# Optimization experiments

Hardware: AMD Instinct MI355X
Metric: run time of the kernel (lower is better)

Reference implementation:

```python
import jax, jax.numpy as jnp
import numpy as np

NEG_SLOPE = 0.2


def gat_conv(x, src, dst, W, att_src, att_dst, bias, heads, out_ch, concat):
    """PyG-style GATConv (eval mode, self-loops already appended to src/dst)."""
    N = x.shape[0]
    h = (x @ W).reshape(N, heads, out_ch)                      # [N,H,C]
    a_src = jnp.einsum('nhc,hc->nh', h, att_src)               # [N,H]
    a_dst = jnp.einsum('nhc,hc->nh', h, att_dst)               # [N,H]
    e = jax.nn.leaky_relu(a_src[src] + a_dst[dst], NEG_SLOPE)  # [E,H]
    # numerically-stable softmax segmented by destination node
    emax = jax.ops.segment_max(e, dst, num_segments=N)         # [N,H]
    e = jnp.exp(e - emax[dst])
    denom = jax.ops.segment_sum(e, dst, num_segments=N)
    alpha = e / (denom[dst] + 1e-16)                           # [E,H]
    msg = h[src] * alpha[..., None]                            # [E,H,C]
    out = jax.ops.segment_sum(msg, dst, num_segments=N)        # [N,H,C]
    out = out.reshape(N, heads * out_ch) if concat else out.mean(axis=1)
    return out + bias


def setup_inputs() -> dict:
    key = jax.random.key(0)
    ks = jax.random.split(key, 9)
    N, E, IN, OUT = 100000, 1600000, 128, 40
    H1, C1 = 8, 8
    x = jax.random.normal(ks[0], (N, IN), dtype=jnp.float32)
    edge_index = jax.random.randint(ks[1], (2, E), 0, N, dtype=jnp.int64)
    s = 0.1
    return {
        'x': x,
        'edge_index': edge_index,
        'W1': jax.random.normal(ks[2], (IN, H1 * C1), dtype=jnp.float32) * s,
        'att_src1': jax.random.normal(ks[3], (H1, C1), dtype=jnp.float32) * s,
        'att_dst1': jax.random.normal(ks[4], (H1, C1), dtype=jnp.float32) * s,
        'b1': jnp.zeros((H1 * C1,), dtype=jnp.float32),
        'W2': jax.random.normal(ks[5], (H1 * C1, OUT), dtype=jnp.float32) * s,
        'att_src2': jax.random.normal(ks[6], (1, OUT), dtype=jnp.float32) * s,
        'att_dst2': jax.random.normal(ks[7], (1, OUT), dtype=jnp.float32) * s,
        'b2': jnp.zeros((OUT,), dtype=jnp.float32),
    }


def reference(x, edge_index, W1, att_src1, att_dst1, b1, W2, att_src2, att_dst2, b2):
    N = x.shape[0]
    loops = jnp.arange(N, dtype=edge_index.dtype)
    src = jnp.concatenate([edge_index[0], loops])  # self-loops (PyG default)
    dst = jnp.concatenate([edge_index[1], loops])
    h = gat_conv(x, src, dst, W1, att_src1, att_dst1, b1, 8, 8, True)
    h = jax.nn.elu(h)  # dropout is identity in eval mode
    out = gat_conv(h, src, dst, W2, att_src2, att_dst2, b2, 1, W2.shape[1], False)
    return jax.nn.log_softmax(out, axis=-1)
```

## Files before the change

kernel.cpp:

```cpp
#include <hip/hip_runtime.h>
#include <math.h>

#define NEG_SLOPE 0.2f
#define BSHIFT 8
#define MAXBUK 512

typedef __attribute__((ext_vector_type(8))) short short8;
typedef __attribute__((ext_vector_type(4))) float floatx4;

static __device__ __forceinline__ float lrelu_exp(float e) {
    e = fmaxf(e, NEG_SLOPE * e);
    return __expf(e);
}

static __device__ __forceinline__ short f2bf(float f) {
    union { float f; unsigned u; } v; v.f = f;
    unsigned r = v.u + 0x7FFFu + ((v.u >> 16) & 1u);
    return (short)(r >> 16);
}
static __device__ __forceinline__ float bf2f(unsigned short s) {
    union { float f; unsigned u; } v;
    v.u = ((unsigned)s) << 16;
    return v.f;
}
static __device__ __forceinline__ float bfpair_lo(unsigned v) {
    union { float f; unsigned u; } x; x.u = v << 16; return x.f;
}
static __device__ __forceinline__ float bfpair_hi(unsigned v) {
    union { float f; unsigned u; } x; x.u = v & 0xffff0000u; return x.f;
}
static __device__ __forceinline__ void splitbf(float f, short& hi, short& lo) {
    hi = f2bf(f);
    lo = f2bf(f - bf2f((unsigned short)hi));
}


__global__ __launch_bounds__(512) void k_hist(const int* __restrict__ dst, int E, int CHUNK,
                                              int NBLK, int NBUK, int* __restrict__ blockhist) {
    __shared__ int hist[MAXBUK];
    int t = threadIdx.x, b = blockIdx.x;
    for (int i = t; i < NBUK; i += 512) hist[i] = 0;
    __syncthreads();
    int e0 = b * CHUNK, e1 = e0 + CHUNK; if (e1 > E) e1 = E;
    for (int e = e0 + t; e < e1; e += 512) atomicAdd(&hist[dst[e] >> BSHIFT], 1);
    __syncthreads();
    for (int i = t; i < NBUK; i += 512) blockhist[(size_t)i * NBLK + b] = hist[i];
}

__global__ __launch_bounds__(256) void k_colscan(int* __restrict__ blockhist,
                                                 int* __restrict__ btot, int NBLK) {
    int bucket = blockIdx.x, t = threadIdx.x;
    int lane = t & 63, wv = t >> 6;
    __shared__ int wsum[4];
    __shared__ int carry_s;
    if (t == 0) carry_s = 0;
    __syncthreads();
    for (int base = 0; base < NBLK; base += 256) {
        int idx = base + t;
        int v = (idx < NBLK) ? blockhist[(size_t)bucket * NBLK + idx] : 0;
        int s = v;
#pragma unroll
        for (int o = 1; o < 64; o <<= 1) {
            int u = __shfl_up(s, o, 64);
            if (lane >= o) s += u;
        }
        if (lane == 63) wsum[wv] = s;
        __syncthreads();
        int b0 = 0;
#pragma unroll
        for (int w = 0; w < 4; ++w) b0 += (w < wv) ? wsum[w] : 0;
        int excl = s + b0 - v + carry_s;
        if (idx < NBLK) blockhist[(size_t)bucket * NBLK + idx] = excl;
        __syncthreads();
        if (t == 255) carry_s += s + b0;
        __syncthreads();
    }
    if (t == 0) btot[bucket] = carry_s;
}

__global__ __launch_bounds__(512) void k_bucket_scan(const int* __restrict__ btot,
                                                     int* __restrict__ bucketbase, int NBUK) {
    __shared__ int sh[512];
    int t = threadIdx.x;
    int v = (t < NBUK) ? btot[t] : 0;
    sh[t] = v;
    __syncthreads();
#pragma unroll
    for (int o = 1; o < 512; o <<= 1) {
        int u = (t >= o) ? sh[t - o] : 0;
        __syncthreads();
        sh[t] += u;
        __syncthreads();
    }
    if (t < NBUK) bucketbase[t] = sh[t] - v;
    if (t == NBUK - 1) bucketbase[NBUK] = sh[t];
}

__global__ __launch_bounds__(512) void k_partition(const int* __restrict__ src,
                                                   const int* __restrict__ dst, int E, int CHUNK,
                                                   int NBLK, int NBUK,
                                                   const int* __restrict__ blockhist,
                                                   const int* __restrict__ bucketbase,
                                                   unsigned* __restrict__ packed) {
    __shared__ int cur[MAXBUK];
    int t = threadIdx.x, b = blockIdx.x;
    for (int i = t; i < NBUK; i += 512)
        cur[i] = blockhist[(size_t)i * NBLK + b] + bucketbase[i];
    __syncthreads();
    int e0 = b * CHUNK, e1 = e0 + CHUNK; if (e1 > E) e1 = E;
    for (int e = e0 + t; e < e1; e += 512) {
        int d = dst[e], s = src[e];
        int pos = atomicAdd(&cur[d >> BSHIFT], 1);
        packed[pos] = ((unsigned)s << 8) | ((unsigned)d & 255u);
    }
}

__global__ __launch_bounds__(256) void k_fine(const unsigned* __restrict__ packed,
                                              const int* __restrict__ bucketbase,
                                              int* __restrict__ offsets,
                                              int* __restrict__ csr_src,
                                              int N, int NBUK) {
    __shared__ int fcnt[256];
    __shared__ int wsum[4];
    int bucket = blockIdx.x, t = threadIdx.x;
    int lo = bucket << BSHIFT;
    int nn = N - lo; if (nn > 256) nn = 256;
    int ebase = bucketbase[bucket];
    int ecnt = bucketbase[bucket + 1] - ebase;
    fcnt[t] = 0;
    __syncthreads();
    for (int i = t; i < ecnt; i += 256) {
        unsigned p = packed[ebase + i];
        atomicAdd(&fcnt[p & 255u], 1);
    }
    __syncthreads();
    int v = fcnt[t];
    int lane = t & 63, wv = t >> 6;
    int s = v;
#pragma unroll
    for (int o = 1; o < 64; o <<= 1) {
        int u = __shfl_up(s, o, 64);
        if (lane >= o) s += u;
    }
    if (lane == 63) wsum[wv] = s;
    __syncthreads();
    int base = 0;
#pragma unroll
    for (int w = 0; w < 4; ++w) base += (w < wv) ? wsum[w] : 0;
    int excl = s + base - v;
    if (t < nn) offsets[lo + t] = ebase + excl;
    if (bucket == NBUK - 1 && t == 0) offsets[N] = ebase + ecnt;
    __syncthreads();
    fcnt[t] = excl;
    __syncthreads();
    for (int i = t; i < ecnt; i += 256) {
        unsigned p = packed[ebase + i];
        int pos = atomicAdd(&fcnt[p & 255u], 1);
        csr_src[ebase + pos] = (int)(p >> 8);
    }
}

__global__ __launch_bounds__(256) void k_splitW2(const float* __restrict__ W2,
                                                 short* __restrict__ w2h,
                                                 short* __restrict__ w2l) {
    int i = blockIdx.x * 256 + threadIdx.x;
    if (i < 64 * 48) {
        int row = i / 48, col = i % 48;
        short hi = 0, lo = 0;
        if (col < 40) splitbf(W2[row * 40 + col], hi, lo);
        w2h[i] = hi; w2l[i] = lo;
    }
}

__global__ __launch_bounds__(256) void k_gemm1(const float* __restrict__ x,
                                               const float* __restrict__ W1,
                                               const float* __restrict__ att_s,
                                               const float* __restrict__ att_d,
                                               unsigned short* __restrict__ h1b,
                                               float* __restrict__ a_s1,
                                               float* __restrict__ a_d1, int N) {
    int tid = threadIdx.x, wave = tid >> 6, lane = tid & 63;
    int n16 = lane & 15, q = lane >> 4;
    int nb = blockIdx.x * 64 + wave * 16;
    if (nb >= N) return;

    short8 bfr[4][4];
#pragma unroll
    for (int ct = 0; ct < 4; ++ct) {
        int n = ct * 16 + n16;
#pragma unroll
        for (int kc = 0; kc < 4; ++kc) {
            int k0 = kc * 32 + q * 8;
            short8 b;
#pragma unroll
            for (int j = 0; j < 8; ++j) b[j] = f2bf(W1[(k0 + j) * 64 + n]);
            bfr[ct][kc] = b;
        }
    }

    int arow = nb + n16; if (arow >= N) arow = N - 1;
    const float* xr = x + (size_t)arow * 128 + q * 8;
    short8 afr[4];
#pragma unroll
    for (int kc = 0; kc < 4; ++kc) {
        float4 u0 = *(const float4*)(xr + kc * 32);
        float4 u1 = *(const float4*)(xr + kc * 32 + 4);
        short8 a;
        a[0] = f2bf(u0.x); a[1] = f2bf(u0.y); a[2] = f2bf(u0.z); a[3] = f2bf(u0.w);
        a[4] = f2bf(u1.x); a[5] = f2bf(u1.y); a[6] = f2bf(u1.z); a[7] = f2bf(u1.w);
        afr[kc] = a;
    }

    floatx4 acc[4];
#pragma unroll
    for (int ct = 0; ct < 4; ++ct) {
        floatx4 c = {0.f, 0.f, 0.f, 0.f};
#pragma unroll
        for (int kc = 0; kc < 4; ++kc)
            c = __builtin_amdgcn_mfma_f32_16x16x32_bf16(afr[kc], bfr[ct][kc], c, 0, 0, 0);
        acc[ct] = c;
    }

#pragma unroll
    for (int ct = 0; ct < 4; ++ct) {
#pragma unroll
        for (int r = 0; r < 4; ++r) {
            int row = nb + q * 4 + r;
            if (row < N) h1b[(size_t)row * 64 + ct * 16 + n16] = (unsigned short)f2bf(acc[ct][r]);
        }
    }

#pragma unroll
    for (int ct = 0; ct < 4; ++ct) {
        float as = att_s[ct * 16 + n16];
        float ad = att_d[ct * 16 + n16];
#pragma unroll
        for (int r = 0; r < 4; ++r) {
            float ps = acc[ct][r] * as;
            float pd = acc[ct][r] * ad;
#pragma unroll
            for (int m = 1; m < 8; m <<= 1) {
                ps += __shfl_xor(ps, m, 64);
                pd += __shfl_xor(pd, m, 64);
            }
            int row = nb + q * 4 + r;
            if ((n16 & 7) == 0 && row < N) {
                int h = 2 * ct + (n16 >> 3);
                a_s1[row * 8 + h] = ps;
                a_d1[row * 8 + h] = pd;
            }
        }
    }
}

__global__ __launch_bounds__(256) void k_agg1(const unsigned short* __restrict__ h1b,
                                              const float* __restrict__ a_s1,
                                              const float* __restrict__ a_d1,
                                              const int* __restrict__ offsets,
                                              const int* __restrict__ csr_src,
                                              const float* __restrict__ b1,
                                              float* __restrict__ y1, int N) {
    int wave = threadIdx.x >> 6, lane = threadIdx.x & 63;
    int q = lane >> 4;
    int ll = lane & 15;
    int d = (blockIdx.x * 4 + wave) * 4 + q;
    bool dvalid = (d < N);
    int de = dvalid ? d : N - 1;
    int g = ll >> 3;
    int c = ll & 7;
    float ad = a_d1[de * 8 + c];
    int i0 = offsets[de];
    int deg = dvalid ? (offsets[de + 1] - i0) : 0;
    int dmax = deg;
    dmax = max(dmax, __shfl_xor(dmax, 16, 64));
    dmax = max(dmax, __shfl_xor(dmax, 32, 64));
    float acc[8] = {0.f, 0.f, 0.f, 0.f, 0.f, 0.f, 0.f, 0.f};
    float wsum_l = 0.f;
    if (g == 0) {
        float w0 = lrelu_exp(a_s1[de * 8 + c] + ad);
        uint4 v = *(const uint4*)(h1b + (size_t)de * 64 + 8 * c);
        acc[0] = w0 * bfpair_lo(v.x); acc[1] = w0 * bfpair_hi(v.x);
        acc[2] = w0 * bfpair_lo(v.y); acc[3] = w0 * bfpair_hi(v.y);
        acc[4] = w0 * bfpair_lo(v.z); acc[5] = w0 * bfpair_hi(v.z);
        acc[6] = w0 * bfpair_lo(v.w); acc[7] = w0 * bfpair_hi(v.w);
        wsum_l = w0;
    }
    for (int j = 0; j < dmax; j += 8) {
        int b0 = i0 + j + 4 * g;
        int idx[4]; bool lv[4];
#pragma unroll
        for (int u = 0; u < 4; ++u) {
            int jj = j + 4 * g + u;
            lv[u] = (jj < deg);
            idx[u] = de;
            if (lv[u]) idx[u] = csr_src[b0 + u];
        }
        float ev[4];
#pragma unroll
        for (int u = 0; u < 4; ++u) ev[u] = a_s1[idx[u] * 8 + c] + ad;
        uint4 vv[4];
#pragma unroll
        for (int u = 0; u < 4; ++u)
            vv[u] = *(const uint4*)(h1b + (size_t)idx[u] * 64 + 8 * c);
#pragma unroll
        for (int u = 0; u < 4; ++u) {
            float w = lv[u] ? lrelu_exp(ev[u]) : 0.f;
            wsum_l += w;
            acc[0] = fmaf(w, bfpair_lo(vv[u].x), acc[0]);
            acc[1] = fmaf(w, bfpair_hi(vv[u].x), acc[1]);
            acc[2] = fmaf(w, bfpair_lo(vv[u].y), acc[2]);
            acc[3] = fmaf(w, bfpair_hi(vv[u].y), acc[3]);
            acc[4] = fmaf(w, bfpair_lo(vv[u].z), acc[4]);
            acc[5] = fmaf(w, bfpair_hi(vv[u].z), acc[5]);
            acc[6] = fmaf(w, bfpair_lo(vv[u].w), acc[6]);
            acc[7] = fmaf(w, bfpair_hi(vv[u].w), acc[7]);
        }
    }
#pragma unroll
    for (int k = 0; k < 8; ++k) acc[k] += __shfl(acc[k], lane + 8, 64);
    wsum_l += __shfl(wsum_l, lane + 8, 64);
    if (g == 0 && dvalid) {
        float inv = 1.f / (wsum_l + 1e-16f);
        float4 bA = *(const float4*)(b1 + 8 * c);
        float4 bB = *(const float4*)(b1 + 8 * c + 4);
        float o[8];
        o[0] = acc[0] * inv + bA.x;
        o[1] = acc[1] * inv + bA.y;
        o[2] = acc[2] * inv + bA.z;
        o[3] = acc[3] * inv + bA.w;
        o[4] = acc[4] * inv + bB.x;
        o[5] = acc[5] * inv + bB.y;
        o[6] = acc[6] * inv + bB.z;
        o[7] = acc[7] * inv + bB.w;
#pragma unroll
        for (int k = 0; k < 8; ++k) o[k] = o[k] > 0.f ? o[k] : (__expf(o[k]) - 1.f);
        float4 s0 = make_float4(o[0], o[1], o[2], o[3]);
        float4 s1 = make_float4(o[4], o[5], o[6], o[7]);
        *(float4*)(y1 + (size_t)d * 64 + 8 * c) = s0;
        *(float4*)(y1 + (size_t)d * 64 + 8 * c + 4) = s1;
    }
}

__global__ __launch_bounds__(256) void k_gemm2(const float* __restrict__ y1,
                                               const short* __restrict__ w2h,
                                               const short* __restrict__ w2l,
                                               const float* __restrict__ att_s,
                                               const float* __restrict__ att_d,
                                               unsigned short* __restrict__ h2b,
                                               float* __restrict__ a2s,
                                               float* __restrict__ a2d, int N) {
    int tid = threadIdx.x, wave = tid >> 6, lane = tid & 63;
    int n16 = lane & 15, q = lane >> 4;
    int nb = blockIdx.x * 64 + wave * 16;
    if (nb >= N) return;

    int arow = nb + n16; if (arow >= N) arow = N - 1;
    const float* yr = y1 + (size_t)arow * 64 + q * 8;
    short8 ah[2], al[2];
#pragma unroll
    for (int kc = 0; kc < 2; ++kc) {
        float4 u0 = *(const float4*)(yr + kc * 32);
        float4 u1 = *(const float4*)(yr + kc * 32 + 4);
        short8 h, l; short hi, lo;
        splitbf(u0.x, hi, lo); h[0] = hi; l[0] = lo;
        splitbf(u0.y, hi, lo); h[1] = hi; l[1] = lo;
        splitbf(u0.z, hi, lo); h[2] = hi; l[2] = lo;
        splitbf(u0.w, hi, lo); h[3] = hi; l[3] = lo;
        splitbf(u1.x, hi, lo); h[4] = hi; l[4] = lo;
        splitbf(u1.y, hi, lo); h[5] = hi; l[5] = lo;
        splitbf(u1.z, hi, lo); h[6] = hi; l[6] = lo;
        splitbf(u1.w, hi, lo); h[7] = hi; l[7] = lo;
        ah[kc] = h; al[kc] = l;
    }

    float psr[4] = {0.f, 0.f, 0.f, 0.f}, pdr[4] = {0.f, 0.f, 0.f, 0.f};
#pragma unroll
    for (int ct = 0; ct < 3; ++ct) {
        int n = ct * 16 + n16;
        short8 bh0, bh1, bl0, bl1;
#pragma unroll
        for (int j = 0; j < 8; ++j) {
            int k0 = q * 8 + j;
            bh0[j] = w2h[k0 * 48 + n];
            bl0[j] = w2l[k0 * 48 + n];
            bh1[j] = w2h[(32 + k0) * 48 + n];
            bl1[j] = w2l[(32 + k0) * 48 + n];
        }
        floatx4 c = {0.f, 0.f, 0.f, 0.f};
        c = __builtin_amdgcn_mfma_f32_16x16x32_bf16(ah[0], bl0, c, 0, 0, 0);
        c = __builtin_amdgcn_mfma_f32_16x16x32_bf16(al[0], bh0, c, 0, 0, 0);
        c = __builtin_amdgcn_mfma_f32_16x16x32_bf16(ah[0], bh0, c, 0, 0, 0);
        c = __builtin_amdgcn_mfma_f32_16x16x32_bf16(ah[1], bl1, c, 0, 0, 0);
        c = __builtin_amdgcn_mfma_f32_16x16x32_bf16(al[1], bh1, c, 0, 0, 0);
        c = __builtin_amdgcn_mfma_f32_16x16x32_bf16(ah[1], bh1, c, 0, 0, 0);

        int col = ct * 16 + n16;
#pragma unroll
        for (int r = 0; r < 4; ++r) {
            int row = nb + q * 4 + r;
            if (col < 40 && row < N) h2b[(size_t)row * 40 + col] = (unsigned short)f2bf(c[r]);
        }
        float asv = (col < 40) ? att_s[col] : 0.f;
        float adv = (col < 40) ? att_d[col] : 0.f;
#pragma unroll
        for (int r = 0; r < 4; ++r) {
            psr[r] = fmaf(c[r], asv, psr[r]);
            pdr[r] = fmaf(c[r], adv, pdr[r]);
        }
    }
#pragma unroll
    for (int r = 0; r < 4; ++r) {
        float ps = psr[r], pd = pdr[r];
#pragma unroll
        for (int m = 1; m < 16; m <<= 1) {
            ps += __shfl_xor(ps, m, 64);
            pd += __shfl_xor(pd, m, 64);
        }
        int row = nb + q * 4 + r;
        if (n16 == 0 && row < N) { a2s[row] = ps; a2d[row] = pd; }
    }
}

__global__ __launch_bounds__(256) void k_agg2(const unsigned short* __restrict__ h2b,
                                              const float* __restrict__ a2s,
                                              const float* __restrict__ a2d,
                                              const int* __restrict__ offsets,
                                              const int* __restrict__ csr_src,
                                              const float* __restrict__ b2,
                                              float* __restrict__ out, int N) {
    int wave = threadIdx.x >> 6, lane = threadIdx.x & 63;
    int q = lane >> 4;
    int ll = lane & 15;
    int d = (blockIdx.x * 4 + wave) * 4 + q;
    bool dvalid = (d < N);
    int de = dvalid ? d : N - 1;
    int g = ll / 5;
    int c = ll - g * 5;
    bool lane_ok = (ll < 15);
    float ad = a2d[de];
    float w0 = lrelu_exp(a2s[de] + ad);
    int i0 = offsets[de];
    int deg = offsets[de + 1] - i0;
    if (!dvalid) deg = 0;
    int dmax = deg;
    dmax = max(dmax, __shfl_xor(dmax, 16, 64));
    dmax = max(dmax, __shfl_xor(dmax, 32, 64));
    float acc[8] = {0.f, 0.f, 0.f, 0.f, 0.f, 0.f, 0.f, 0.f};
    float wsum_l = 0.f;
    if (g == 0) {
        uint4 v = *(const uint4*)(h2b + (size_t)de * 40 + 8 * c);
        acc[0] = w0 * bfpair_lo(v.x); acc[1] = w0 * bfpair_hi(v.x);
        acc[2] = w0 * bfpair_lo(v.y); acc[3] = w0 * bfpair_hi(v.y);
        acc[4] = w0 * bfpair_lo(v.z); acc[5] = w0 * bfpair_hi(v.z);
        acc[6] = w0 * bfpair_lo(v.w); acc[7] = w0 * bfpair_hi(v.w);
    }
    for (int j = 0; j < dmax; j += 12) {
        int b0 = i0 + j + 4 * g;
        int idx[4]; bool lv[4];
#pragma unroll
        for (int u = 0; u < 4; ++u) {
            int jj = j + 4 * g + u;
            lv[u] = lane_ok && (jj < deg);
            idx[u] = de;
            if (lv[u]) idx[u] = csr_src[b0 + u];
        }
        float ev[4];
#pragma unroll
        for (int u = 0; u < 4; ++u) ev[u] = a2s[idx[u]] + ad;
        uint4 vv[4];
#pragma unroll
        for (int u = 0; u < 4; ++u)
            vv[u] = *(const uint4*)(h2b + (size_t)idx[u] * 40 + 8 * c);
#pragma unroll
        for (int u = 0; u < 4; ++u) {
            float w = lv[u] ? lrelu_exp(ev[u]) : 0.f;
            if (c == 0) wsum_l += w;
            acc[0] = fmaf(w, bfpair_lo(vv[u].x), acc[0]);
            acc[1] = fmaf(w, bfpair_hi(vv[u].x), acc[1]);
            acc[2] = fmaf(w, bfpair_lo(vv[u].y), acc[2]);
            acc[3] = fmaf(w, bfpair_hi(vv[u].y), acc[3]);
            acc[4] = fmaf(w, bfpair_lo(vv[u].z), acc[4]);
            acc[5] = fmaf(w, bfpair_hi(vv[u].z), acc[5]);
            acc[6] = fmaf(w, bfpair_lo(vv[u].w), acc[6]);
            acc[7] = fmaf(w, bfpair_hi(vv[u].w), acc[7]);
        }
    }
#pragma unroll
    for (int k = 0; k < 8; ++k)
        acc[k] += __shfl(acc[k], lane + 5, 64) + __shfl(acc[k], lane + 10, 64);
    wsum_l += __shfl(wsum_l, lane + 5, 64) + __shfl(wsum_l, lane + 10, 64);
    wsum_l = __shfl(wsum_l, lane & 48, 64);
    float wsum = wsum_l + w0;
    bool act5 = (ll < 5) && dvalid;
    float inv = 1.f / (wsum + 1e-16f);
    float4 bA = *(const float4*)(b2 + 8 * c);
    float4 bB = *(const float4*)(b2 + 8 * c + 4);
    float o[8];
    o[0] = acc[0] * inv + bA.x;
    o[1] = acc[1] * inv + bA.y;
    o[2] = acc[2] * inv + bA.z;
    o[3] = acc[3] * inv + bA.w;
    o[4] = acc[4] * inv + bB.x;
    o[5] = acc[5] * inv + bB.y;
    o[6] = acc[6] * inv + bB.z;
    o[7] = acc[7] * inv + bB.w;
    float mxl = -INFINITY;
    if (act5) {
        mxl = fmaxf(fmaxf(fmaxf(o[0], o[1]), fmaxf(o[2], o[3])),
                    fmaxf(fmaxf(o[4], o[5]), fmaxf(o[6], o[7])));
    }
#pragma unroll
    for (int mm = 1; mm < 8; mm <<= 1) mxl = fmaxf(mxl, __shfl_xor(mxl, mm, 64));
    float exl = 0.f;
    if (act5) {
#pragma unroll
        for (int k = 0; k < 8; ++k) exl += __expf(o[k] - mxl);
    }
#pragma unroll
    for (int mm = 1; mm < 8; mm <<= 1) exl += __shfl_xor(exl, mm, 64);
    if (act5) {
        float lse = mxl + __logf(exl);
        float4 s0 = make_float4(o[0] - lse, o[1] - lse, o[2] - lse, o[3] - lse);
        float4 s1 = make_float4(o[4] - lse, o[5] - lse, o[6] - lse, o[7] - lse);
        *(float4*)(out + (size_t)d * 40 + 8 * c) = s0;
        *(float4*)(out + (size_t)d * 40 + 8 * c + 4) = s1;
    }
}


extern "C" void kernel_launch(void* const* d_in, const int* in_sizes, int n_in,
                              void* d_out, int out_size, void* d_ws, size_t ws_size,
                              hipStream_t stream) {
    const float* x   = (const float*)d_in[0];
    const int*   ei  = (const int*)d_in[1];
    const float* W1  = (const float*)d_in[2];
    const float* as1 = (const float*)d_in[3];
    const float* ad1 = (const float*)d_in[4];
    const float* b1  = (const float*)d_in[5];
    const float* W2  = (const float*)d_in[6];
    const float* as2 = (const float*)d_in[7];
    const float* ad2 = (const float*)d_in[8];
    const float* b2  = (const float*)d_in[9];
    float* out = (float*)d_out;

    int N = in_sizes[0] / 128;
    int E = in_sizes[1] / 2;
    const int* src = ei;
    const int* dst = ei + E;

    int NBUK = (N + 255) >> BSHIFT;
    int CHUNK = 4096;
    int NBLK = (E + CHUNK - 1) / CHUNK;

    char* ws = (char*)d_ws;
    size_t off = 0;
    auto alloc = [&](size_t bytes) -> char* {
        char* p = ws + off;
        off += (bytes + 255) & ~(size_t)255;
        return p;
    };
    unsigned short* h1b = (unsigned short*)alloc((size_t)N * 64 * 2);
    float* a_s1    = (float*)alloc((size_t)N * 8 * 4);
    float* a_d1    = (float*)alloc((size_t)N * 8 * 4);
    float* y1      = (float*)alloc((size_t)N * 64 * 4);
    size_t shared_sz = (size_t)N * 40 * 2;
    if ((size_t)E * 4 > shared_sz) shared_sz = (size_t)E * 4;
    char*  region  = alloc(shared_sz);
    unsigned short* h2b = (unsigned short*)region;
    unsigned* packed    = (unsigned*)region;
    float* a2s     = (float*)alloc((size_t)N * 4);
    float* a2d     = (float*)alloc((size_t)N * 4);
    int*   offsets = (int*)alloc((size_t)(N + 1) * 4);
    int*   csr_src = (int*)alloc((size_t)E * 4);
    int*   blockhist  = (int*)alloc((size_t)NBUK * NBLK * 4);
    int*   btot       = (int*)alloc((size_t)NBUK * 4);
    int*   bucketbase = (int*)alloc((size_t)(NBUK + 1) * 4);
    short* w2h     = (short*)alloc((size_t)64 * 48 * 2);
    short* w2l     = (short*)alloc((size_t)64 * 48 * 2);

    int nb1 = (N + 15) / 16;
    int nb2 = (N + 15) / 16;
    int gb = (N + 63) / 64;

    k_hist<<<NBLK, 512, 0, stream>>>(dst, E, CHUNK, NBLK, NBUK, blockhist);
    k_colscan<<<NBUK, 256, 0, stream>>>(blockhist, btot, NBLK);
    k_bucket_scan<<<1, 512, 0, stream>>>(btot, bucketbase, NBUK);
    k_partition<<<NBLK, 512, 0, stream>>>(src, dst, E, CHUNK, NBLK, NBUK, blockhist,
                                          bucketbase, packed);
    k_fine<<<NBUK, 256, 0, stream>>>(packed, bucketbase, offsets, csr_src, N, NBUK);
    k_splitW2<<<12, 256, 0, stream>>>(W2, w2h, w2l);
    k_gemm1<<<gb, 256, 0, stream>>>(x, W1, as1, ad1, h1b, a_s1, a_d1, N);
    k_agg1<<<nb1, 256, 0, stream>>>(h1b, a_s1, a_d1, offsets, csr_src, b1, y1, N);
    k_gemm2<<<gb, 256, 0, stream>>>(y1, w2h, w2l, as2, ad2, h2b, a2s, a2d, N);
    k_agg2<<<nb2, 256, 0, stream>>>(h2b, a2s, a2d, offsets, csr_src, b2, out, N);
}
```

Baseline: 169.7 us.

## Prefetch next CSR indices in aggregation loops and remap agg1 to 8 lanes per node

In both aggregation kernels, the neighbor indices for the next iteration are loaded while the current feature gathers are in flight, so the dependent index-to-gather load chain is software-pipelined. In agg1 each destination node now uses 8 lanes instead of 16 and handles 8 edges per iteration in one lane group. This removes the cross-half shuffle reduction and covers twice as many nodes per block. The cost is more registers per thread (8 prefetched indices plus 8 uint4 gathers), which may lower occupancy.

```diff
diff --git a/kernel.cpp b/kernel.cpp
--- a/kernel.cpp
+++ b/kernel.cpp
@@ -261,51 +261,49 @@
                                               const float* __restrict__ b1,
                                               float* __restrict__ y1, int N) {
     int wave = threadIdx.x >> 6, lane = threadIdx.x & 63;
-    int q = lane >> 4;
-    int ll = lane & 15;
-    int d = (blockIdx.x * 4 + wave) * 4 + q;
+    int oct = lane >> 3;
+    int c = lane & 7;
+    int d = (blockIdx.x * 4 + wave) * 8 + oct;
     bool dvalid = (d < N);
     int de = dvalid ? d : N - 1;
-    int g = ll >> 3;
-    int c = ll & 7;
     float ad = a_d1[de * 8 + c];
     int i0 = offsets[de];
     int deg = dvalid ? (offsets[de + 1] - i0) : 0;
     int dmax = deg;
-    dmax = max(dmax, __shfl_xor(dmax, 16, 64));
-    dmax = max(dmax, __shfl_xor(dmax, 32, 64));
-    float acc[8] = {0.f, 0.f, 0.f, 0.f, 0.f, 0.f, 0.f, 0.f};
-    float wsum_l = 0.f;
-    if (g == 0) {
-        float w0 = lrelu_exp(a_s1[de * 8 + c] + ad);
-        uint4 v = *(const uint4*)(h1b + (size_t)de * 64 + 8 * c);
-        acc[0] = w0 * bfpair_lo(v.x); acc[1] = w0 * bfpair_hi(v.x);
-        acc[2] = w0 * bfpair_lo(v.y); acc[3] = w0 * bfpair_hi(v.y);
-        acc[4] = w0 * bfpair_lo(v.z); acc[5] = w0 * bfpair_hi(v.z);
-        acc[6] = w0 * bfpair_lo(v.w); acc[7] = w0 * bfpair_hi(v.w);
-        wsum_l = w0;
+#pragma unroll
+    for (int mm = 8; mm < 64; mm <<= 1) dmax = max(dmax, __shfl_xor(dmax, mm, 64));
+    float w0 = lrelu_exp(a_s1[de * 8 + c] + ad);
+    uint4 v0 = *(const uint4*)(h1b + (size_t)de * 64 + 8 * c);
+    float acc[8];
+    acc[0] = w0 * bfpair_lo(v0.x); acc[1] = w0 * bfpair_hi(v0.x);
+    acc[2] = w0 * bfpair_lo(v0.y); acc[3] = w0 * bfpair_hi(v0.y);
+    acc[4] = w0 * bfpair_lo(v0.z); acc[5] = w0 * bfpair_hi(v0.z);
+    acc[6] = w0 * bfpair_lo(v0.w); acc[7] = w0 * bfpair_hi(v0.w);
+    float wsum = w0;
+    int idxA[8];
+#pragma unroll
+    for (int u = 0; u < 8; ++u) {
+        idxA[u] = de;
+        if (u < deg) idxA[u] = csr_src[i0 + u];
     }
     for (int j = 0; j < dmax; j += 8) {
-        int b0 = i0 + j + 4 * g;
-        int idx[4]; bool lv[4];
-#pragma unroll
-        for (int u = 0; u < 4; ++u) {
-            int jj = j + 4 * g + u;
-            lv[u] = (jj < deg);
-            idx[u] = de;
-            if (lv[u]) idx[u] = csr_src[b0 + u];
-        }
-        float ev[4];
-#pragma unroll
-        for (int u = 0; u < 4; ++u) ev[u] = a_s1[idx[u] * 8 + c] + ad;
-        uint4 vv[4];
-#pragma unroll
-        for (int u = 0; u < 4; ++u)
-            vv[u] = *(const uint4*)(h1b + (size_t)idx[u] * 64 + 8 * c);
-#pragma unroll
-        for (int u = 0; u < 4; ++u) {
-            float w = lv[u] ? lrelu_exp(ev[u]) : 0.f;
-            wsum_l += w;
+        float ev[8]; uint4 vv[8];
+#pragma unroll
+        for (int u = 0; u < 8; ++u) ev[u] = a_s1[idxA[u] * 8 + c];
+#pragma unroll
+        for (int u = 0; u < 8; ++u)
+            vv[u] = *(const uint4*)(h1b + (size_t)idxA[u] * 64 + 8 * c);
+        int idxB[8];
+#pragma unroll
+        for (int u = 0; u < 8; ++u) {
+            int jj = j + 8 + u;
+            idxB[u] = de;
+            if (jj < deg) idxB[u] = csr_src[i0 + jj];
+        }
+#pragma unroll
+        for (int u = 0; u < 8; ++u) {
+            float w = (j + u < deg) ? lrelu_exp(ev[u] + ad) : 0.f;
+            wsum += w;
             acc[0] = fmaf(w, bfpair_lo(vv[u].x), acc[0]);
             acc[1] = fmaf(w, bfpair_hi(vv[u].x), acc[1]);
             acc[2] = fmaf(w, bfpair_lo(vv[u].y), acc[2]);
@@ -315,12 +313,11 @@
             acc[6] = fmaf(w, bfpair_lo(vv[u].w), acc[6]);
             acc[7] = fmaf(w, bfpair_hi(vv[u].w), acc[7]);
         }
-    }
-#pragma unroll
-    for (int k = 0; k < 8; ++k) acc[k] += __shfl(acc[k], lane + 8, 64);
-    wsum_l += __shfl(wsum_l, lane + 8, 64);
-    if (g == 0 && dvalid) {
-        float inv = 1.f / (wsum_l + 1e-16f);
+#pragma unroll
+        for (int u = 0; u < 8; ++u) idxA[u] = idxB[u];
+    }
+    if (dvalid) {
+        float inv = 1.f / (wsum + 1e-16f);
         float4 bA = *(const float4*)(b1 + 8 * c);
         float4 bB = *(const float4*)(b1 + 8 * c + 4);
         float o[8];
@@ -454,26 +451,31 @@
         acc[4] = w0 * bfpair_lo(v.z); acc[5] = w0 * bfpair_hi(v.z);
         acc[6] = w0 * bfpair_lo(v.w); acc[7] = w0 * bfpair_hi(v.w);
     }
+    int idxA[4];
+#pragma unroll
+    for (int u = 0; u < 4; ++u) {
+        int jj = 4 * g + u;
+        idxA[u] = de;
+        if (lane_ok && jj < deg) idxA[u] = csr_src[i0 + jj];
+    }
     for (int j = 0; j < dmax; j += 12) {
-        int b0 = i0 + j + 4 * g;
-        int idx[4]; bool lv[4];
+        float ev[4]; uint4 vv[4];
+#pragma unroll
+        for (int u = 0; u < 4; ++u) ev[u] = a2s[idxA[u]];
+#pragma unroll
+        for (int u = 0; u < 4; ++u)
+            vv[u] = *(const uint4*)(h2b + (size_t)idxA[u] * 40 + 8 * c);
+        int idxB[4];
+#pragma unroll
+        for (int u = 0; u < 4; ++u) {
+            int jj = j + 12 + 4 * g + u;
+            idxB[u] = de;
+            if (lane_ok && jj < deg) idxB[u] = csr_src[i0 + jj];
+        }
 #pragma unroll
         for (int u = 0; u < 4; ++u) {
             int jj = j + 4 * g + u;
-            lv[u] = lane_ok && (jj < deg);
-            idx[u] = de;
-            if (lv[u]) idx[u] = csr_src[b0 + u];
-        }
-        float ev[4];
-#pragma unroll
-        for (int u = 0; u < 4; ++u) ev[u] = a2s[idx[u]] + ad;
-        uint4 vv[4];
-#pragma unroll
-        for (int u = 0; u < 4; ++u)
-            vv[u] = *(const uint4*)(h2b + (size_t)idx[u] * 40 + 8 * c);
-#pragma unroll
-        for (int u = 0; u < 4; ++u) {
-            float w = lv[u] ? lrelu_exp(ev[u]) : 0.f;
+            float w = (lane_ok && jj < deg) ? lrelu_exp(ev[u] + ad) : 0.f;
             if (c == 0) wsum_l += w;
             acc[0] = fmaf(w, bfpair_lo(vv[u].x), acc[0]);
             acc[1] = fmaf(w, bfpair_hi(vv[u].x), acc[1]);
@@ -484,6 +486,8 @@
             acc[6] = fmaf(w, bfpair_lo(vv[u].w), acc[6]);
             acc[7] = fmaf(w, bfpair_hi(vv[u].w), acc[7]);
         }
+#pragma unroll
+        for (int u = 0; u < 4; ++u) idxA[u] = idxB[u];
     }
 #pragma unroll
     for (int k = 0; k < 8; ++k)
@@ -578,7 +582,7 @@
     short* w2h     = (short*)alloc((size_t)64 * 48 * 2);
     short* w2l     = (short*)alloc((size_t)64 * 48 * 2);
 
-    int nb1 = (N + 15) / 16;
+    int nb1 = (N + 31) / 32;
     int nb2 = (N + 15) / 16;
     int gb = (N + 63) / 64;
 
```

Result: no change. 170.8 us (+0.7%).
